# Kernel tuning notes

Measured on AMD Instinct MI355X. Metric: run time of the kernel, lower is better.

The kernel has to match this reference:

```python
import jax, jax.numpy as jnp
import numpy as np

EPS = 1e-5
DIM = 128
SCALE = DIM ** (-0.5)


def setup_inputs() -> dict:
    key = jax.random.key(0)
    k1, k2, k3 = jax.random.split(key, 3)
    B, N, D = 2, 128 * 128, DIM
    Q = N // 4
    x = jax.random.normal(k1, (B, N, D), dtype=jnp.float32)
    gamma = jnp.ones((D,), dtype=jnp.float32)
    beta = jnp.zeros((D,), dtype=jnp.float32)
    queries = jax.random.normal(k2, (Q, D), dtype=jnp.float32)
    W = jax.random.normal(k3, (2 * D, D), dtype=jnp.float32) * (1.0 / np.sqrt(D))
    return {"x": x, "gamma": gamma, "beta": beta, "queries": queries, "W": W}


def reference(x, gamma, beta, queries, W):
    # LayerNorm over last dim (eps matches torch default 1e-5)
    mu = jnp.mean(x, axis=-1, keepdims=True)
    var = jnp.mean(jnp.square(x - mu), axis=-1, keepdims=True)
    xn = (x - mu) * jax.lax.rsqrt(var + EPS) * gamma + beta  # [B, N, D]
    # learned-query cross attention: sim = Q @ xn^T * scale -> softmax -> @ xn
    sim = jnp.einsum('qd,bnd->bqn', queries, xn) * SCALE     # [B, Q, N]
    attn = jax.nn.softmax(sim, axis=-1)
    out = jnp.einsum('bqn,bnd->bqd', attn, xn)               # [B, Q, D]
    # trailing linear: dim -> 2*dim, no bias
    return jnp.einsum('bqd,ed->bqe', out, W)                 # [B, Q, 2D]
```

## Files before the change

kernel.cpp:

```cpp
#include <hip/hip_runtime.h>
#include <stdint.h>

#define Nn 16384
#define Dd 128
#define Qq 4096
#define Ee 256
#define KV 64

typedef __bf16 bf16x8 __attribute__((ext_vector_type(8)));
typedef float floatx16 __attribute__((ext_vector_type(16)));
typedef unsigned uintx2 __attribute__((ext_vector_type(2)));

__device__ __forceinline__ float fexp2(float x) {
#if __has_builtin(__builtin_amdgcn_exp2f)
  return __builtin_amdgcn_exp2f(x);
#else
  return exp2f(x);
#endif
}
__device__ __forceinline__ unsigned pk_bf(float lo, float hi) {
  return __builtin_amdgcn_perm(__float_as_uint(hi) + 0x8000u,
                               __float_as_uint(lo) + 0x8000u, 0x07060302u);
}
__device__ __forceinline__ void stage16(const void* g, void* lds_uniform) {
  __builtin_amdgcn_global_load_lds(
      (const __attribute__((address_space(1))) unsigned int*)g,
      (__attribute__((address_space(3))) unsigned int*)lds_uniform, 16, 0, 0);
}
__device__ __forceinline__ void plswap(unsigned a, unsigned b, int hi,
                                       unsigned& r0, unsigned& r1) {
#if __has_builtin(__builtin_amdgcn_permlane32_swap)
  uintx2 r = __builtin_amdgcn_permlane32_swap(a, b, false, false);
  r0 = r[0];
  r1 = r[1];
  (void)hi;
#else
  unsigned ax = __shfl_xor(a, 32);
  unsigned bx = __shfl_xor(b, 32);
  r0 = hi ? bx : a;
  r1 = hi ? b : ax;
#endif
}

__global__ __launch_bounds__(256) void k_lnt(
    const float* __restrict__ x, const float* __restrict__ gamma,
    const float* __restrict__ beta, const float* __restrict__ queries,
    const float* __restrict__ W, unsigned* __restrict__ xn,
    unsigned short* __restrict__ xnT, unsigned short* __restrict__ qb,
    unsigned short* __restrict__ wb) {
  __shared__ __align__(16) uint2 lds2[64 * 32];
  const int tid = threadIdx.x;
  const int bid = blockIdx.x;
  const int b = bid >> 8, n0 = (bid & 255) * 64;
  const int r = tid >> 2, qd = tid & 3;

  const float4* xp = (const float4*)(x + ((size_t)(b * Nn + n0 + r)) * Dd + qd * 32);
  float4 v[8];
  float s = 0.f, s2 = 0.f;
#pragma unroll
  for (int i = 0; i < 8; ++i) {
    v[i] = xp[i];
    s += (v[i].x + v[i].y) + (v[i].z + v[i].w);
    s2 += (v[i].x * v[i].x + v[i].y * v[i].y) + (v[i].z * v[i].z + v[i].w * v[i].w);
  }
  s += __shfl_xor(s, 1); s2 += __shfl_xor(s2, 1);
  s += __shfl_xor(s, 2); s2 += __shfl_xor(s2, 2);
  float mu = s * (1.0f / 128.0f);
  float var = s2 * (1.0f / 128.0f) - mu * mu;
  float rs = rsqrtf(var + 1e-5f);

  const float4* gp = (const float4*)(gamma + qd * 32);
  const float4* bp = (const float4*)(beta + qd * 32);
  unsigned pk[16];
#pragma unroll
  for (int i = 0; i < 8; ++i) {
    float4 g = gp[i], bt = bp[i];
    pk[2 * i] = pk_bf((v[i].x - mu) * rs * g.x + bt.x, (v[i].y - mu) * rs * g.y + bt.y);
    pk[2 * i + 1] = pk_bf((v[i].z - mu) * rs * g.z + bt.z, (v[i].w - mu) * rs * g.w + bt.w);
  }
  unsigned* xrow = xn + ((size_t)(b * Nn + n0 + r)) * 64;
#pragma unroll
  for (int j = 0; j < 4; ++j)
    *(uint4*)(xrow + (((qd * 4 + j) ^ (r & 7)) * 4)) =
        make_uint4(pk[4 * j], pk[4 * j + 1], pk[4 * j + 2], pk[4 * j + 3]);
  const int rk = r & 31;
#pragma unroll
  for (int kk = 0; kk < 8; ++kk)
    lds2[r * 32 + ((qd * 8 + kk) ^ rk)] = make_uint2(pk[2 * kk], pk[2 * kk + 1]);
  __syncthreads();
  const int dq = tid >> 3, nc = tid & 7;
  uint2 U[8];
#pragma unroll
  for (int j = 0; j < 8; ++j) {
    int rr = nc * 8 + j;
    U[j] = lds2[rr * 32 + (dq ^ (rr & 31))];
  }
#pragma unroll
  for (int e = 0; e < 4; ++e) {
    int d = dq * 4 + e;
    unsigned a0 = (e & 2) ? U[0].y : U[0].x, a1 = (e & 2) ? U[1].y : U[1].x;
    unsigned a2 = (e & 2) ? U[2].y : U[2].x, a3 = (e & 2) ? U[3].y : U[3].x;
    unsigned a4 = (e & 2) ? U[4].y : U[4].x, a5 = (e & 2) ? U[5].y : U[5].x;
    unsigned a6 = (e & 2) ? U[6].y : U[6].x, a7 = (e & 2) ? U[7].y : U[7].x;
    unsigned sel = (e & 1) ? 0x07060302u : 0x05040100u;
    uint4 o;
    o.x = __builtin_amdgcn_perm(a1, a0, sel);
    o.y = __builtin_amdgcn_perm(a3, a2, sel);
    o.z = __builtin_amdgcn_perm(a5, a4, sel);
    o.w = __builtin_amdgcn_perm(a7, a6, sel);
    *(uint4*)(xnT + ((size_t)(b * Dd + d)) * Nn + n0 + (nc ^ (d & 7)) * 8) = o;
  }
  const float QSC = 0.08838834764831845f * 1.4426950408889634f;
  const int total4 = (Qq * Dd + Ee * Dd) / 4;
  for (int u = bid * 256 + tid; u < total4; u += 512 * 256) {
    if (u < Qq * Dd / 4) {
      float4 v4 = ((const float4*)queries)[u];
      ((uint2*)qb)[u] = make_uint2(pk_bf(v4.x * QSC, v4.y * QSC),
                                   pk_bf(v4.z * QSC, v4.w * QSC));
    } else {
      float4 v4 = ((const float4*)W)[u - Qq * Dd / 4];
      ((uint2*)wb)[u - Qq * Dd / 4] =
          make_uint2(pk_bf(v4.x, v4.y), pk_bf(v4.z, v4.w));
    }
  }
}

template <int NS, int NWAVE>
__global__ __launch_bounds__(NWAVE * 64, 2) void k_attn(
    const unsigned short* __restrict__ xn,
    const unsigned short* __restrict__ xnT,
    const unsigned short* __restrict__ qb,
    float* __restrict__ o_part,
    float* __restrict__ l_part) {
  constexpr int NCH = Nn / NS;
  constexpr int NIT = NCH / KV;
  constexpr int QT = Qq / (32 * NWAVE);
  constexpr int CPW = 16 / NWAVE;
  __shared__ __align__(16) char lds_x[2][16384];
  __shared__ __align__(16) char lds_xt[3][16384];

  const int bid = blockIdx.x;
  const int split = bid % NS;
  const int qt = (bid / NS) % QT;
  const int b = bid / (NS * QT);
  const int tid = threadIdx.x;
  const int wave = tid >> 6, lane = tid & 63;
  const int col = lane & 31, half = lane >> 5;
  const int ck = col & 7;
  const int qwbase = qt * (32 * NWAVE) + wave * 32;

  bf16x8 qf[8];
#pragma unroll
  for (int s = 0; s < 8; ++s)
    qf[s] = *(const bf16x8*)(qb + (size_t)(qwbase + col) * Dd + s * 16 + half * 8);

  const floatx16 fz = {0.f,0.f,0.f,0.f,0.f,0.f,0.f,0.f,0.f,0.f,0.f,0.f,0.f,0.f,0.f,0.f};
  floatx16 O[4];
#pragma unroll
  for (int d = 0; d < 4; ++d) O[d] = fz;
  float lsum = 0.f;

  const char* gx = (const char*)xn + (size_t)b * Nn * 256;
  const char* gxt = (const char*)xnT + (size_t)b * Dd * Nn * 2;
  const int tbase = split * (NCH / KV);

  auto stgX = [&](int t, int buf) {
    const char* xsrc = gx + (size_t)(tbase + t) * (KV * 256);
#pragma unroll
    for (int p = 0; p < CPW; ++p) {
      int m = wave * CPW + p;
      stage16(xsrc + m * 1024 + lane * 16, &lds_x[buf][0] + m * 1024);
    }
  };
  auto stgXT = [&](int t, int buf) {
#pragma unroll
    for (int p = 0; p < CPW; ++p) {
      int m = wave * CPW + p;
      const char* g = gxt + (size_t)(m * 8 + (lane >> 3)) * (Nn * 2) +
                      (size_t)(tbase + t) * (KV * 2) + (lane & 7) * 16;
      stage16(g, &lds_xt[buf][0] + m * 1024);
    }
  };
  auto sread = [&](const char* lx, int mt, int s) {
    return *(const bf16x8*)(lx + (32 * mt + col) * 256 +
                            (((2 * s + half) ^ ck) * 16));
  };
  auto exp_mt = [&](const floatx16& S, unsigned Pm[4][2]) {
#pragma unroll
    for (int t = 0; t < 4; ++t) {
      float p0 = fexp2(S[4 * t]);
      float p1 = fexp2(S[4 * t + 1]);
      float p2 = fexp2(S[4 * t + 2]);
      float p3 = fexp2(S[4 * t + 3]);
      lsum += (p0 + p1) + (p2 + p3);
      Pm[t][0] = pk_bf(p0, p1);
      Pm[t][1] = pk_bf(p2, p3);
    }
  };
  auto pv_s2 = [&](const char* lxt, unsigned (&P)[2][4][2], int s2) {
    const int mt = s2 >> 1, ge = 2 * (s2 & 1), go = ge + 1;
    unsigned w0, w1, w2, w3;
    plswap(P[mt][ge][0], P[mt][go][0], half, w0, w2);
    plswap(P[mt][ge][1], P[mt][go][1], half, w1, w3);
    union { uint4 u; bf16x8 v; } ap;
    ap.u = make_uint4(w0, w1, w2, w3);
#pragma unroll
    for (int dn = 0; dn < 4; ++dn) {
      bf16x8 bx = *(const bf16x8*)(lxt + (32 * dn + col) * 128 +
                                   (((2 * s2 + half) ^ ck) * 16));
      O[dn] = __builtin_amdgcn_mfma_f32_32x32x16_bf16(ap.v, bx, O[dn], 0, 0, 0);
    }
  };

  int xt_prev = 0;

  auto body = [&](int i, unsigned (&Pprev)[2][4][2], unsigned (&Pcur)[2][4][2]) {
    if (i + 1 < NIT) {
      asm volatile("s_waitcnt vmcnt(8)" ::: "memory");
    } else {
      asm volatile("s_waitcnt vmcnt(0)" ::: "memory");
    }
    __builtin_amdgcn_s_barrier();
    __builtin_amdgcn_sched_barrier(0);

    const char* lx = &lds_x[i & 1][0];
    const char* lxt = &lds_xt[xt_prev][0];

    floatx16 S0 = fz;
    __builtin_amdgcn_s_setprio(1);
#pragma unroll
    for (int s = 0; s < 8; ++s)
      S0 = __builtin_amdgcn_mfma_f32_32x32x16_bf16(sread(lx, 0, s), qf[s], S0, 0, 0, 0);
    pv_s2(lxt, Pprev, 0);
    pv_s2(lxt, Pprev, 1);
    __builtin_amdgcn_s_setprio(0);
    exp_mt(S0, Pcur[0]);

    floatx16 S1 = fz;
    __builtin_amdgcn_s_setprio(1);
#pragma unroll
    for (int s = 0; s < 8; ++s)
      S1 = __builtin_amdgcn_mfma_f32_32x32x16_bf16(sread(lx, 1, s), qf[s], S1, 0, 0, 0);
    pv_s2(lxt, Pprev, 2);
    pv_s2(lxt, Pprev, 3);
    __builtin_amdgcn_s_setprio(0);
    exp_mt(S1, Pcur[1]);

    asm volatile("" ::: "memory");
    __builtin_amdgcn_s_barrier();
    if (i + 2 < NIT) {
      stgX(i + 2, i & 1);
      stgXT(i + 2, xt_prev);
    }
    xt_prev = (xt_prev == 2) ? 0 : xt_prev + 1;
  };

  stgX(0, 0); stgXT(0, 0);
  stgX(1, 1); stgXT(1, 1);
  asm volatile("s_waitcnt vmcnt(8)" ::: "memory");
  __builtin_amdgcn_s_barrier();
  __builtin_amdgcn_sched_barrier(0);

  unsigned PA[2][4][2], PB[2][4][2];
  {
    floatx16 S0 = fz, S1 = fz;
    __builtin_amdgcn_s_setprio(1);
#pragma unroll
    for (int s = 0; s < 8; ++s)
      S0 = __builtin_amdgcn_mfma_f32_32x32x16_bf16(sread(&lds_x[0][0], 0, s), qf[s], S0, 0, 0, 0);
#pragma unroll
    for (int s = 0; s < 8; ++s)
      S1 = __builtin_amdgcn_mfma_f32_32x32x16_bf16(sread(&lds_x[0][0], 1, s), qf[s], S1, 0, 0, 0);
    __builtin_amdgcn_s_setprio(0);
    exp_mt(S0, PA[0]);
    exp_mt(S1, PA[1]);
  }
  asm volatile("" ::: "memory");
  __builtin_amdgcn_s_barrier();
  if (NIT > 2) { stgX(2, 0); stgXT(2, 2); }

#pragma unroll 1
  for (int i = 1; i + 1 < NIT; i += 2) {
    body(i, PA, PB);
    body(i + 1, PB, PA);
  }
  body(NIT - 1, PA, PB);
  pv_s2(&lds_xt[xt_prev][0], PB, 0);
  pv_s2(&lds_xt[xt_prev][0], PB, 1);
  pv_s2(&lds_xt[xt_prev][0], PB, 2);
  pv_s2(&lds_xt[xt_prev][0], PB, 3);

  float lt = lsum + __shfl_xor(lsum, 32);
  if (half == 0)
    l_part[(size_t)(b * NS + split) * Qq + qwbase + col] = lt;
  float* op = o_part + ((size_t)(b * NS + split) * Qq + qwbase) * Dd;
#pragma unroll
  for (int dn = 0; dn < 4; ++dn)
#pragma unroll
    for (int r = 0; r < 16; ++r) {
      int q = (r & 3) + 8 * (r >> 2) + 4 * half;
      op[(size_t)q * Dd + dn * 32 + col] = O[dn][r];
    }
}

template <int NS>
__global__ __launch_bounds__(256) void k_comb(
    const float* __restrict__ o_part, const float* __restrict__ l_part,
    const unsigned short* __restrict__ wb, float* __restrict__ out) {
  __shared__ __align__(16) char lds_a[32 * 256];
  __shared__ float lds_linv[32];
  const int bid = blockIdx.x;
  const int b = bid >> 7, qc = bid & 127;
  const int qbase = qc * 32;
  const int tid = threadIdx.x;
  const int wave = tid >> 6, lane = tid & 63;
  const int col = lane & 31, half = lane >> 5;
  const int ck = col & 7;

  if (tid < 32) {
    float l = 0.f;
#pragma unroll
    for (int s = 0; s < NS; ++s)
      l += l_part[(size_t)(b * NS + s) * Qq + qbase + tid];
    lds_linv[tid] = 1.0f / l;
  }
  __syncthreads();

#pragma unroll
  for (int i = 0; i < 4; ++i) {
    int idx = i * 256 + tid;
    int q = idx >> 5, d4 = idx & 31;
    float4 acc = make_float4(0.f, 0.f, 0.f, 0.f);
#pragma unroll
    for (int s = 0; s < NS; ++s) {
      float4 v = *(const float4*)(o_part + ((size_t)(b * NS + s) * Qq + qbase + q) * Dd + d4 * 4);
      acc.x += v.x; acc.y += v.y; acc.z += v.z; acc.w += v.w;
    }
    float li = lds_linv[q];
    int w = d4 >> 1;
    int pos = (w & 8) | ((w ^ (q & 7)) & 7);
    *(uint2*)(lds_a + q * 256 + pos * 16 + (d4 & 1) * 8) =
        make_uint2(pk_bf(acc.x * li, acc.y * li), pk_bf(acc.z * li, acc.w * li));
  }
  __syncthreads();

  bf16x8 af[8];
#pragma unroll
  for (int s = 0; s < 8; ++s) {
    int u = 2 * s + half;
    int pos = (u & 8) | ((u ^ ck) & 7);
    af[s] = *(const bf16x8*)(lds_a + col * 256 + pos * 16);
  }

  const floatx16 fz = {0.f,0.f,0.f,0.f,0.f,0.f,0.f,0.f,0.f,0.f,0.f,0.f,0.f,0.f,0.f,0.f};
#pragma unroll
  for (int et = 0; et < 2; ++et) {
    floatx16 C = fz;
    int e_row = wave * 64 + et * 32 + col;
#pragma unroll
    for (int s = 0; s < 8; ++s) {
      bf16x8 bw = *(const bf16x8*)(wb + (size_t)e_row * Dd + s * 16 + half * 8);
      C = __builtin_amdgcn_mfma_f32_32x32x16_bf16(af[s], bw, C, 0, 0, 0);
    }
#pragma unroll
    for (int r = 0; r < 16; ++r) {
      int q = qbase + (r & 3) + 8 * (r >> 2) + 4 * half;
      out[((size_t)b * Qq + q) * Ee + wave * 64 + et * 32 + col] = C[r];
    }
  }
}

extern "C" void kernel_launch(void* const* d_in, const int* in_sizes, int n_in,
                              void* d_out, int out_size, void* d_ws, size_t ws_size,
                              hipStream_t stream) {
  const float* x = (const float*)d_in[0];
  const float* gamma = (const float*)d_in[1];
  const float* beta = (const float*)d_in[2];
  const float* queries = (const float*)d_in[3];
  const float* W = (const float*)d_in[4];
  float* out = (float*)d_out;

  char* w = (char*)d_ws;
  unsigned* xn = (unsigned*)(w);
  unsigned short* xnT = (unsigned short*)(w + 8388608);
  unsigned short* qb = (unsigned short*)(w + 16777216);
  unsigned short* wb = (unsigned short*)(w + 17825792);
  float* o_part = (float*)(w + 17891328);
  float* l_part = (float*)(w + 51445760);

  k_lnt<<<dim3(512), dim3(256), 0, stream>>>(x, gamma, beta, queries, W,
                                             xn, xnT, qb, wb);
  k_attn<8, 4><<<dim3(512), dim3(256), 0, stream>>>((const unsigned short*)xn,
                                                    xnT, qb, o_part, l_part);
  k_comb<8><<<dim3(256), dim3(256), 0, stream>>>(o_part, l_part, wb, out);
}
```

Baseline: 159.7 us.

## Drop transposed xn copy; use LDS transpose reads and retune split/waves

```diff
diff --git a/kernel.cpp b/kernel.cpp
--- a/kernel.cpp
+++ b/kernel.cpp
@@ -41,20 +41,24 @@
   r1 = hi ? b : ax;
 #endif
 }
+__device__ __forceinline__ uintx2 tr16(const char* p) {
+  unsigned a = (unsigned)(size_t)(const __attribute__((address_space(3))) char*)p;
+  uintx2 r;
+  asm volatile("ds_read_b64_tr_b16 %0, %1" : "=v"(r) : "v"(a));
+  return r;
+}
 
 __global__ __launch_bounds__(256) void k_lnt(
     const float* __restrict__ x, const float* __restrict__ gamma,
     const float* __restrict__ beta, const float* __restrict__ queries,
     const float* __restrict__ W, unsigned* __restrict__ xn,
-    unsigned short* __restrict__ xnT, unsigned short* __restrict__ qb,
-    unsigned short* __restrict__ wb) {
-  __shared__ __align__(16) uint2 lds2[64 * 32];
+    unsigned short* __restrict__ qb, unsigned short* __restrict__ wb) {
   const int tid = threadIdx.x;
   const int bid = blockIdx.x;
-  const int b = bid >> 8, n0 = (bid & 255) * 64;
+  const int b = bid >> 8, t = bid & 255;
   const int r = tid >> 2, qd = tid & 3;
 
-  const float4* xp = (const float4*)(x + ((size_t)(b * Nn + n0 + r)) * Dd + qd * 32);
+  const float4* xp = (const float4*)(x + ((size_t)(b * Nn + t * 64 + r)) * Dd + qd * 32);
   float4 v[8];
   float s = 0.f, s2 = 0.f;
 #pragma unroll
@@ -78,38 +82,13 @@
     pk[2 * i] = pk_bf((v[i].x - mu) * rs * g.x + bt.x, (v[i].y - mu) * rs * g.y + bt.y);
     pk[2 * i + 1] = pk_bf((v[i].z - mu) * rs * g.z + bt.z, (v[i].w - mu) * rs * g.w + bt.w);
   }
-  unsigned* xrow = xn + ((size_t)(b * Nn + n0 + r)) * 64;
-#pragma unroll
-  for (int j = 0; j < 4; ++j)
-    *(uint4*)(xrow + (((qd * 4 + j) ^ (r & 7)) * 4)) =
-        make_uint4(pk[4 * j], pk[4 * j + 1], pk[4 * j + 2], pk[4 * j + 3]);
-  const int rk = r & 31;
-#pragma unroll
-  for (int kk = 0; kk < 8; ++kk)
-    lds2[r * 32 + ((qd * 8 + kk) ^ rk)] = make_uint2(pk[2 * kk], pk[2 * kk + 1]);
-  __syncthreads();
-  const int dq = tid >> 3, nc = tid & 7;
-  uint2 U[8];
-#pragma unroll
-  for (int j = 0; j < 8; ++j) {
-    int rr = nc * 8 + j;
-    U[j] = lds2[rr * 32 + (dq ^ (rr & 31))];
-  }
-#pragma unroll
-  for (int e = 0; e < 4; ++e) {
-    int d = dq * 4 + e;
-    unsigned a0 = (e & 2) ? U[0].y : U[0].x, a1 = (e & 2) ? U[1].y : U[1].x;
-    unsigned a2 = (e & 2) ? U[2].y : U[2].x, a3 = (e & 2) ? U[3].y : U[3].x;
-    unsigned a4 = (e & 2) ? U[4].y : U[4].x, a5 = (e & 2) ? U[5].y : U[5].x;
-    unsigned a6 = (e & 2) ? U[6].y : U[6].x, a7 = (e & 2) ? U[7].y : U[7].x;
-    unsigned sel = (e & 1) ? 0x07060302u : 0x05040100u;
-    uint4 o;
-    o.x = __builtin_amdgcn_perm(a1, a0, sel);
-    o.y = __builtin_amdgcn_perm(a3, a2, sel);
-    o.z = __builtin_amdgcn_perm(a5, a4, sel);
-    o.w = __builtin_amdgcn_perm(a7, a6, sel);
-    *(uint4*)(xnT + ((size_t)(b * Dd + d)) * Nn + n0 + (nc ^ (d & 7)) * 8) = o;
-  }
+  unsigned* tb = xn + ((size_t)(b * 256 + t)) * 4096;
+  const int base = (r >> 2) * 256 + (r & 3) * 8;
+  *(uint4*)(tb + base + (2 * qd) * 32) = make_uint4(pk[0], pk[1], pk[2], pk[3]);
+  *(uint4*)(tb + base + (2 * qd) * 32 + 4) = make_uint4(pk[4], pk[5], pk[6], pk[7]);
+  *(uint4*)(tb + base + (2 * qd + 1) * 32) = make_uint4(pk[8], pk[9], pk[10], pk[11]);
+  *(uint4*)(tb + base + (2 * qd + 1) * 32 + 4) = make_uint4(pk[12], pk[13], pk[14], pk[15]);
+
   const float QSC = 0.08838834764831845f * 1.4426950408889634f;
   const int total4 = (Qq * Dd + Ee * Dd) / 4;
   for (int u = bid * 256 + tid; u < total4; u += 512 * 256) {
@@ -128,7 +107,6 @@
 template <int NS, int NWAVE>
 __global__ __launch_bounds__(NWAVE * 64, 2) void k_attn(
     const unsigned short* __restrict__ xn,
-    const unsigned short* __restrict__ xnT,
     const unsigned short* __restrict__ qb,
     float* __restrict__ o_part,
     float* __restrict__ l_part) {
@@ -136,8 +114,7 @@
   constexpr int NIT = NCH / KV;
   constexpr int QT = Qq / (32 * NWAVE);
   constexpr int CPW = 16 / NWAVE;
-  __shared__ __align__(16) char lds_x[2][16384];
-  __shared__ __align__(16) char lds_xt[3][16384];
+  __shared__ __align__(16) char lds_x[3][16384];
 
   const int bid = blockIdx.x;
   const int split = bid % NS;
@@ -146,7 +123,6 @@
   const int tid = threadIdx.x;
   const int wave = tid >> 6, lane = tid & 63;
   const int col = lane & 31, half = lane >> 5;
-  const int ck = col & 7;
   const int qwbase = qt * (32 * NWAVE) + wave * 32;
 
   bf16x8 qf[8];
@@ -160,30 +136,27 @@
   for (int d = 0; d < 4; ++d) O[d] = fz;
   float lsum = 0.f;
 
-  const char* gx = (const char*)xn + (size_t)b * Nn * 256;
-  const char* gxt = (const char*)xnT + (size_t)b * Dd * Nn * 2;
-  const int tbase = split * (NCH / KV);
+  const char* gx = (const char*)xn + (size_t)b * 256 * 16384;
+  const int tbase = split * NIT;
+  const int soff = (col >> 2) * 1024 + (col & 3) * 32 + half * 16;
+  const int pvoff = 2 * half * 1024 + (col >> 4) * 128 + (col & 15) * 8;
 
   auto stgX = [&](int t, int buf) {
-    const char* xsrc = gx + (size_t)(tbase + t) * (KV * 256);
+    const char* src = gx + (size_t)(tbase + t) * 16384;
 #pragma unroll
     for (int p = 0; p < CPW; ++p) {
       int m = wave * CPW + p;
-      stage16(xsrc + m * 1024 + lane * 16, &lds_x[buf][0] + m * 1024);
-    }
-  };
-  auto stgXT = [&](int t, int buf) {
-#pragma unroll
-    for (int p = 0; p < CPW; ++p) {
-      int m = wave * CPW + p;
-      const char* g = gxt + (size_t)(m * 8 + (lane >> 3)) * (Nn * 2) +
-                      (size_t)(tbase + t) * (KV * 2) + (lane & 7) * 16;
-      stage16(g, &lds_xt[buf][0] + m * 1024);
-    }
-  };
-  auto sread = [&](const char* lx, int mt, int s) {
-    return *(const bf16x8*)(lx + (32 * mt + col) * 256 +
-                            (((2 * s + half) ^ ck) * 16));
+      stage16(src + m * 1024 + lane * 16, &lds_x[buf][0] + m * 1024);
+    }
+  };
+  auto sphase = [&](const char* lx, floatx16* S) {
+#pragma unroll
+    for (int s = 0; s < 8; ++s)
+#pragma unroll
+      for (int mt = 0; mt < 2; ++mt) {
+        bf16x8 ax = *(const bf16x8*)(lx + soff + mt * 8192 + s * 128);
+        S[mt] = __builtin_amdgcn_mfma_f32_32x32x16_bf16(ax, qf[s], S[mt], 0, 0, 0);
+      }
   };
   auto exp_mt = [&](const floatx16& S, unsigned Pm[4][2]) {
 #pragma unroll
@@ -204,80 +177,74 @@
     plswap(P[mt][ge][1], P[mt][go][1], half, w1, w3);
     union { uint4 u; bf16x8 v; } ap;
     ap.u = make_uint4(w0, w1, w2, w3);
-#pragma unroll
-    for (int dn = 0; dn < 4; ++dn) {
-      bf16x8 bx = *(const bf16x8*)(lxt + (32 * dn + col) * 128 +
-                                   (((2 * s2 + half) ^ ck) * 16));
-      O[dn] = __builtin_amdgcn_mfma_f32_32x32x16_bf16(ap.v, bx, O[dn], 0, 0, 0);
-    }
-  };
-
-  int xt_prev = 0;
+    const char* ab = lxt + pvoff + s2 * 4096;
+    uintx2 t0a = tr16(ab);           uintx2 t0b = tr16(ab + 1024);
+    uintx2 t1a = tr16(ab + 256);     uintx2 t1b = tr16(ab + 256 + 1024);
+    uintx2 t2a = tr16(ab + 512);     uintx2 t2b = tr16(ab + 512 + 1024);
+    uintx2 t3a = tr16(ab + 768);     uintx2 t3b = tr16(ab + 768 + 1024);
+    asm volatile("s_waitcnt lgkmcnt(0)" ::);
+    __builtin_amdgcn_sched_barrier(0);
+    union { uint4 u; bf16x8 v; } bx;
+    bx.u = make_uint4(t0a[0], t0a[1], t0b[0], t0b[1]);
+    O[0] = __builtin_amdgcn_mfma_f32_32x32x16_bf16(ap.v, bx.v, O[0], 0, 0, 0);
+    bx.u = make_uint4(t1a[0], t1a[1], t1b[0], t1b[1]);
+    O[1] = __builtin_amdgcn_mfma_f32_32x32x16_bf16(ap.v, bx.v, O[1], 0, 0, 0);
+    bx.u = make_uint4(t2a[0], t2a[1], t2b[0], t2b[1]);
+    O[2] = __builtin_amdgcn_mfma_f32_32x32x16_bf16(ap.v, bx.v, O[2], 0, 0, 0);
+    bx.u = make_uint4(t3a[0], t3a[1], t3b[0], t3b[1]);
+    O[3] = __builtin_amdgcn_mfma_f32_32x32x16_bf16(ap.v, bx.v, O[3], 0, 0, 0);
+  };
+
+  int prev = 0, cur = 1;
 
   auto body = [&](int i, unsigned (&Pprev)[2][4][2], unsigned (&Pcur)[2][4][2]) {
     if (i + 1 < NIT) {
-      asm volatile("s_waitcnt vmcnt(8)" ::: "memory");
+      asm volatile("s_waitcnt vmcnt(2)" ::: "memory");
     } else {
       asm volatile("s_waitcnt vmcnt(0)" ::: "memory");
     }
     __builtin_amdgcn_s_barrier();
     __builtin_amdgcn_sched_barrier(0);
 
-    const char* lx = &lds_x[i & 1][0];
-    const char* lxt = &lds_xt[xt_prev][0];
-
-    floatx16 S0 = fz;
+    const char* lx = &lds_x[cur][0];
+    const char* lxt = &lds_x[prev][0];
+
+    floatx16 S[2]; S[0] = fz; S[1] = fz;
     __builtin_amdgcn_s_setprio(1);
-#pragma unroll
-    for (int s = 0; s < 8; ++s)
-      S0 = __builtin_amdgcn_mfma_f32_32x32x16_bf16(sread(lx, 0, s), qf[s], S0, 0, 0, 0);
+    sphase(lx, S);
     pv_s2(lxt, Pprev, 0);
     pv_s2(lxt, Pprev, 1);
-    __builtin_amdgcn_s_setprio(0);
-    exp_mt(S0, Pcur[0]);
-
-    floatx16 S1 = fz;
-    __builtin_amdgcn_s_setprio(1);
-#pragma unroll
-    for (int s = 0; s < 8; ++s)
-      S1 = __builtin_amdgcn_mfma_f32_32x32x16_bf16(sread(lx, 1, s), qf[s], S1, 0, 0, 0);
     pv_s2(lxt, Pprev, 2);
     pv_s2(lxt, Pprev, 3);
     __builtin_amdgcn_s_setprio(0);
-    exp_mt(S1, Pcur[1]);
+    exp_mt(S[0], Pcur[0]);
+    exp_mt(S[1], Pcur[1]);
 
     asm volatile("" ::: "memory");
     __builtin_amdgcn_s_barrier();
-    if (i + 2 < NIT) {
-      stgX(i + 2, i & 1);
-      stgXT(i + 2, xt_prev);
-    }
-    xt_prev = (xt_prev == 2) ? 0 : xt_prev + 1;
-  };
-
-  stgX(0, 0); stgXT(0, 0);
-  stgX(1, 1); stgXT(1, 1);
-  asm volatile("s_waitcnt vmcnt(8)" ::: "memory");
+    if (i + 2 < NIT) stgX(i + 2, prev);
+    int nxt = (cur == 2) ? 0 : cur + 1;
+    prev = cur; cur = nxt;
+  };
+
+  stgX(0, 0);
+  stgX(1, 1);
+  asm volatile("s_waitcnt vmcnt(2)" ::: "memory");
   __builtin_amdgcn_s_barrier();
   __builtin_amdgcn_sched_barrier(0);
 
   unsigned PA[2][4][2], PB[2][4][2];
   {
-    floatx16 S0 = fz, S1 = fz;
+    floatx16 S[2]; S[0] = fz; S[1] = fz;
     __builtin_amdgcn_s_setprio(1);
-#pragma unroll
-    for (int s = 0; s < 8; ++s)
-      S0 = __builtin_amdgcn_mfma_f32_32x32x16_bf16(sread(&lds_x[0][0], 0, s), qf[s], S0, 0, 0, 0);
-#pragma unroll
-    for (int s = 0; s < 8; ++s)
-      S1 = __builtin_amdgcn_mfma_f32_32x32x16_bf16(sread(&lds_x[0][0], 1, s), qf[s], S1, 0, 0, 0);
+    sphase(&lds_x[0][0], S);
     __builtin_amdgcn_s_setprio(0);
-    exp_mt(S0, PA[0]);
-    exp_mt(S1, PA[1]);
+    exp_mt(S[0], PA[0]);
+    exp_mt(S[1], PA[1]);
   }
   asm volatile("" ::: "memory");
   __builtin_amdgcn_s_barrier();
-  if (NIT > 2) { stgX(2, 0); stgXT(2, 2); }
+  if (NIT > 2) stgX(2, 2);
 
 #pragma unroll 1
   for (int i = 1; i + 1 < NIT; i += 2) {
@@ -285,10 +252,10 @@
     body(i + 1, PB, PA);
   }
   body(NIT - 1, PA, PB);
-  pv_s2(&lds_xt[xt_prev][0], PB, 0);
-  pv_s2(&lds_xt[xt_prev][0], PB, 1);
-  pv_s2(&lds_xt[xt_prev][0], PB, 2);
-  pv_s2(&lds_xt[xt_prev][0], PB, 3);
+  pv_s2(&lds_x[prev][0], PB, 0);
+  pv_s2(&lds_x[prev][0], PB, 1);
+  pv_s2(&lds_x[prev][0], PB, 2);
+  pv_s2(&lds_x[prev][0], PB, 3);
 
   float lt = lsum + __shfl_xor(lsum, 32);
   if (half == 0)
@@ -382,15 +349,14 @@
 
   char* w = (char*)d_ws;
   unsigned* xn = (unsigned*)(w);
-  unsigned short* xnT = (unsigned short*)(w + 8388608);
-  unsigned short* qb = (unsigned short*)(w + 16777216);
-  unsigned short* wb = (unsigned short*)(w + 17825792);
-  float* o_part = (float*)(w + 17891328);
-  float* l_part = (float*)(w + 51445760);
+  unsigned short* qb = (unsigned short*)(w + 8388608);
+  unsigned short* wb = (unsigned short*)(w + 9437184);
+  float* o_part = (float*)(w + 9502720);
+  float* l_part = (float*)(w + 9502720 + 67108864);
 
   k_lnt<<<dim3(512), dim3(256), 0, stream>>>(x, gamma, beta, queries, W,
-                                             xn, xnT, qb, wb);
-  k_attn<8, 4><<<dim3(512), dim3(256), 0, stream>>>((const unsigned short*)xn,
-                                                    xnT, qb, o_part, l_part);
-  k_comb<8><<<dim3(256), dim3(256), 0, stream>>>(o_part, l_part, wb, out);
-}
+                                             xn, qb, wb);
+  k_attn<16, 8><<<dim3(512), dim3(512), 0, stream>>>(
+      (const unsigned short*)xn, qb, o_part, l_part);
+  k_comb<16><<<dim3(256), dim3(256), 0, stream>>>(o_part, l_part, wb, out);
+}
```

After: 171.9 us. 1.08x slower.
